# Kernel optimization log

Measured on AMD Instinct MI355X. Metric: run time of the kernel, lower is better.

The kernel has to match this reference:

```python
import jax, jax.numpy as jnp
import numpy as np

DIM = 1024
HEADS = 16
HEAD_DIM = DIM // HEADS
MLP_HID = 4 * DIM
LN_EPS = 1e-5


def layer_norm(x, g, b):
    mu = jnp.mean(x, axis=-1, keepdims=True)
    var = jnp.mean((x - mu) ** 2, axis=-1, keepdims=True)
    return (x - mu) * jax.lax.rsqrt(var + LN_EPS) * g + b


def setup_inputs() -> dict:
    key = jax.random.key(0)
    ks = jax.random.split(key, 8)
    s = 0.02
    return {
        "x": jax.random.normal(ks[0], (8, 1024, DIM), dtype=jnp.float32),
        "attention_mask": jnp.ones((8, 1024), dtype=jnp.int32),
        "ln1_g": jnp.ones((DIM,), jnp.float32),
        "ln1_b": jnp.zeros((DIM,), jnp.float32),
        "qkv_w": jax.random.normal(ks[1], (3 * DIM, DIM), jnp.float32) * s,
        "proj_w": jax.random.normal(ks[2], (DIM, DIM), jnp.float32) * s,
        "proj_b": jnp.zeros((DIM,), jnp.float32),
        "ln2_g": jnp.ones((DIM,), jnp.float32),
        "ln2_b": jnp.zeros((DIM,), jnp.float32),
        "fc1_w": jax.random.normal(ks[3], (MLP_HID, DIM), jnp.float32) * s,
        "fc1_b": jnp.zeros((MLP_HID,), jnp.float32),
        "fc2_w": jax.random.normal(ks[4], (DIM, MLP_HID), jnp.float32) * s,
        "fc2_b": jnp.zeros((DIM,), jnp.float32),
    }


def reference(x, attention_mask, ln1_g, ln1_b, qkv_w, proj_w, proj_b,
              ln2_g, ln2_b, fc1_w, fc1_b, fc2_w, fc2_b):
    B, N, C = x.shape
    scale = HEAD_DIM ** -0.5

    # --- attention branch ---
    h = layer_norm(x, ln1_g, ln1_b)
    qkv = h @ qkv_w.T                       # [B,N,3C] (no qkv bias)
    qkv = qkv.reshape(B, N, 3, HEADS, HEAD_DIM).transpose(2, 0, 3, 1, 4)
    q, k, v = qkv[0], qkv[1], qkv[2]        # each [B,H,N,Dh]
    attn = jnp.einsum('bhnd,bhmd->bhnm', q, k) * scale
    mask = (attention_mask == 0)[:, None, None, :]  # [B,1,1,N]
    attn = jnp.where(mask, -jnp.inf, attn)
    attn = jax.nn.softmax(attn, axis=-1)
    out = jnp.einsum('bhnm,bhmd->bhnd', attn, v)
    out = out.transpose(0, 2, 1, 3).reshape(B, N, C)
    out = out @ proj_w.T + proj_b
    x = x + out

    # --- MLP branch ---
    h = layer_norm(x, ln2_g, ln2_b)
    h = jax.nn.gelu(h @ fc1_w.T + fc1_b, approximate=False)
    h = h @ fc2_w.T + fc2_b
    return x + h
```

## Files before the change

### kernel.cpp

```cpp
#include <hip/hip_runtime.h>
#include <hip/hip_bf16.h>
#include <stdint.h>
#include <math.h>

#define DIMC 1024
#define SEQ 1024
#define NBATCH 8
#define NHEADS 16
#define HDIM 64
#define MLPHID 4096
#define NROWS (NBATCH*SEQ)

typedef __attribute__((ext_vector_type(8))) short short8;
typedef __attribute__((ext_vector_type(4))) float f32x4;
typedef __attribute__((ext_vector_type(16))) float f32x16;
typedef __attribute__((ext_vector_type(4))) unsigned int u32x4;

__device__ __forceinline__ short f2bf(float f) {
  union { float f; uint32_t u; } x; x.f = f;
  uint32_t r = (x.u + 0x7FFFu + ((x.u >> 16) & 1u)) >> 16;
  return (short)r;
}

__device__ __forceinline__ unsigned int pk2(float lo, float hi_) {
  return ((unsigned int)(unsigned short)f2bf(hi_) << 16) |
          (unsigned int)(unsigned short)f2bf(lo);
}

__device__ __forceinline__ float gelu_f(float v) {
  const float t = v * v;
  const float p = fmaf(t, 0.044715f, 1.0f);
  const float e = exp2f(2.3022082f * v * p);
  return v - v * __builtin_amdgcn_rcpf(e + 1.0f);
}

__device__ __forceinline__ f32x4 mfma16(short8 a, short8 b, f32x4 c) {
  return __builtin_amdgcn_mfma_f32_16x16x32_bf16(a, b, c, 0, 0, 0);
}
__device__ __forceinline__ f32x16 mfma32(short8 a, short8 b, f32x16 c) {
  return __builtin_amdgcn_mfma_f32_32x32x16_bf16(a, b, c, 0, 0, 0);
}

__device__ __forceinline__ void gload16(const void* g, void* l) {
  __builtin_amdgcn_global_load_lds(
      (const __attribute__((address_space(1))) uint32_t*)g,
      (__attribute__((address_space(3))) uint32_t*)l, 16, 0, 0);
}

__global__ __launch_bounds__(256)
void f2bw_kernel(const float* __restrict__ w0, const float* __restrict__ w1,
                 const float* __restrict__ w2, const float* __restrict__ w3,
                 short* __restrict__ o0, short* __restrict__ o1,
                 short* __restrict__ o2, short* __restrict__ o3) {
  const int i = blockIdx.x * 256 + threadIdx.x;
  const float4* src;
  short4* dst;
  if (i < 786432)       { src = (const float4*)w0 + i;             dst = (short4*)o0 + i; }
  else if (i < 1048576) { src = (const float4*)w1 + (i - 786432);  dst = (short4*)o1 + (i - 786432); }
  else if (i < 2097152) { src = (const float4*)w2 + (i - 1048576); dst = (short4*)o2 + (i - 1048576); }
  else                  { src = (const float4*)w3 + (i - 2097152); dst = (short4*)o3 + (i - 2097152); }
  const float4 v = *src;
  short4 o;
  o.x = f2bf(v.x); o.y = f2bf(v.y); o.z = f2bf(v.z); o.w = f2bf(v.w);
  *dst = o;
}

__global__ __launch_bounds__(256)
void ln_kernel(const float* __restrict__ x, const float* __restrict__ g,
               const float* __restrict__ beta, short* __restrict__ out) {
  const int row = blockIdx.x;
  const int tid = threadIdx.x;
  const float4 v = ((const float4*)(x + (size_t)row * DIMC))[tid];
  float s = v.x + v.y + v.z + v.w;
  float q = v.x*v.x + v.y*v.y + v.z*v.z + v.w*v.w;
#pragma unroll
  for (int o = 32; o > 0; o >>= 1) { s += __shfl_down(s, o); q += __shfl_down(q, o); }
  __shared__ float rs[4], rq[4];
  const int lane = tid & 63, w = tid >> 6;
  if (lane == 0) { rs[w] = s; rq[w] = q; }
  __syncthreads();
  s = rs[0] + rs[1] + rs[2] + rs[3];
  q = rq[0] + rq[1] + rq[2] + rq[3];
  const float mean = s * (1.0f / DIMC);
  const float var = q * (1.0f / DIMC) - mean * mean;
  const float rstd = rsqrtf(var + 1e-5f);
  const float4 gv = ((const float4*)g)[tid];
  const float4 bv = ((const float4*)beta)[tid];
  short4 o4;
  o4.x = f2bf((v.x - mean) * rstd * gv.x + bv.x);
  o4.y = f2bf((v.y - mean) * rstd * gv.y + bv.y);
  o4.z = f2bf((v.z - mean) * rstd * gv.z + bv.z);
  o4.w = f2bf((v.w - mean) * rstd * gv.w + bv.w);
  ((short4*)(out + (size_t)row * DIMC))[tid] = o4;
}


#define NOVM ((void)0)
#define NOST ((void)0)
#define VMC4 asm volatile("s_waitcnt vmcnt(4)" ::: "memory")
#define VMC2 asm volatile("s_waitcnt vmcnt(2)" ::: "memory")

#define SA(DB, H, T) \
  gload16(sA0 + (H)*hstep + (size_t)(T)*64, stb + ((DB)*4 + (H))*16384); \
  gload16(sA1 + (H)*hstep + (size_t)(T)*64, stb + ((DB)*4 + (H))*16384 + 8192)

#define SB(DB, H, T) \
  gload16(sB0 + (H)*hstep + (size_t)(T)*64, stb + ((DB)*4 + 2 + (H))*16384); \
  gload16(sB1 + (H)*hstep + (size_t)(T)*64, stb + ((DB)*4 + 2 + (H))*16384 + 8192)

#define PH(DB, QA, QB, LDA, LDB, STAGE, VM) \
  do { \
    if (LDA) { \
      _Pragma("unroll") \
      for (int mi = 0; mi < 4; ++mi) { \
        _Pragma("unroll") \
        for (int ks = 0; ks < 2; ++ks) \
          af[mi][ks] = *(const short8*)(ard##DB + (((QA)*4 + mi)*2 + ks)*1024); \
      } \
    } \
    if (LDB) { \
      _Pragma("unroll") \
      for (int ni = 0; ni < 2; ++ni) { \
        _Pragma("unroll") \
        for (int ks = 0; ks < 2; ++ks) \
          bfv[QB][ni][ks] = *(const short8*)(brd##DB + (((QB)*2 + ni)*2 + ks)*1024); \
      } \
    } \
    STAGE; \
    __builtin_amdgcn_s_barrier(); \
    asm volatile("s_waitcnt lgkmcnt(0)" ::: "memory"); \
    __builtin_amdgcn_sched_barrier(0); \
    __builtin_amdgcn_s_setprio(1); \
    _Pragma("unroll") \
    for (int ks = 0; ks < 2; ++ks) { \
      _Pragma("unroll") \
      for (int mi = 0; mi < 4; ++mi) { \
        _Pragma("unroll") \
        for (int ni = 0; ni < 2; ++ni) \
          acc[(QA)*4 + mi][(QB)*2 + ni] = \
            mfma16(af[mi][ks], bfv[QB][ni][ks], acc[(QA)*4 + mi][(QB)*2 + ni]); \
      } \
    } \
    __builtin_amdgcn_s_setprio(0); \
    VM; \
    __builtin_amdgcn_s_barrier(); \
  } while (0)

template<bool BIAS, bool GELU, bool RESID, bool OBF16>
__global__ __launch_bounds__(512)
void gemm8p(const short* __restrict__ A, const short* __restrict__ W,
            const float* __restrict__ bias, const float* __restrict__ resid,
            float* __restrict__ outF, short* __restrict__ outB,
            int M, int N, int K, int ntl, int mt8)
{
  __shared__ __align__(16) char lsm[131072];
  const int tid = threadIdx.x;
  const int lane = tid & 63;
  const int w = tid >> 6;
  const int wm = w >> 2;
  const int wn = w & 3;
  const int fr = lane & 15;
  const int fko = (lane >> 4) << 3;

  const int bid = blockIdx.x;
  const int xcd = bid & 7, l = bid >> 3;
  const int bm = (xcd * mt8 + l / ntl) << 8;
  const int bn = (l % ntl) << 8;

  int row_[2], kk_[2];
#pragma unroll
  for (int j = 0; j < 2; ++j) {
    const int s = j * 8 + (tid >> 6);
    const int r16 = (tid & 63) >> 2;
    const int cb = ((tid & 3) << 4) ^ (((tid >> 5) & 1) << 5);
    row_[j] = (s >> 1) * 16 + r16;
    kk_[j]  = (s & 1) * 32 + (cb >> 1);
  }
  const short* sA0 = A + (size_t)(bm + row_[0]) * K + kk_[0];
  const short* sA1 = A + (size_t)(bm + row_[1]) * K + kk_[1];
  const short* sB0 = W + (size_t)(bn + row_[0]) * K + kk_[0];
  const short* sB1 = W + (size_t)(bn + row_[1]) * K + kk_[1];
  const size_t hstep = (size_t)128 * K;
  char* stb = lsm + tid * 16;

  const int lofs = fr * 64 + ((fko << 1) ^ (((fr >> 3) & 1) << 5));
  const char* ard0 = lsm + wm * 16384 + lofs;
  const char* brd0 = lsm + 32768 + (wn >> 1) * 16384 + (wn & 1) * 8192 + lofs;
  const char* ard1 = ard0 + 65536;
  const char* brd1 = brd0 + 65536;

  short8 af[4][2];
  short8 bfv[2][2][2];
  f32x4 acc[8][4] = {};

  SA(0, 0, 0); SA(0, 1, 0);
  SB(0, 0, 0); SB(0, 1, 0);
  SB(1, 0, 1); SB(1, 1, 1);
  VMC4;
  __builtin_amdgcn_s_barrier();

  const int nk = K >> 6;
  const int nit = nk >> 1;
  const int tmask = nk - 1;
  for (int it = 0; it < nit; ++it) {
    const int t1 = 2 * it + 1;
    const int t2 = (2 * it + 2) & tmask;
    const int t3 = (2 * it + 3) & tmask;
    PH(0, 0, 0, 1, 1, SA(1, 0, t1), NOVM);
    PH(0, 0, 1, 0, 1, SA(1, 1, t1), NOVM);
    PH(0, 1, 1, 1, 0, SB(0, 0, t2), NOVM);
    PH(0, 1, 0, 0, 0, SB(0, 1, t2), VMC4);
    PH(1, 0, 0, 1, 1, SA(0, 0, t2), NOVM);
    PH(1, 0, 1, 0, 1, SA(0, 1, t2), NOVM);
    PH(1, 1, 1, 1, 0, SB(1, 0, t3), NOVM);
    PH(1, 1, 0, 0, 0, SB(1, 1, t3), VMC4);
  }

  asm volatile("s_waitcnt vmcnt(0)" ::: "memory");
  __builtin_amdgcn_s_barrier();

  const int orow0 = bm + wm * 128 + ((lane >> 4) << 2);
  const int ocol0 = bn + wn * 64 + fr;
#pragma unroll
  for (int mi = 0; mi < 8; ++mi) {
#pragma unroll
    for (int r = 0; r < 4; ++r) {
      const int row = orow0 + mi * 16 + r;
      const size_t base = (size_t)row * N;
#pragma unroll
      for (int ni = 0; ni < 4; ++ni) {
        const int col = ocol0 + ni * 16;
        float v = acc[mi][ni][r];
        if (BIAS) v += bias[col];
        if (GELU) v = gelu_f(v);
        if (RESID) v += resid[base + col];
        if (OBF16) outB[base + col] = f2bf(v);
        else       outF[base + col] = v;
      }
    }
  }
}

#define SA2(DB, H, T) \
  gload16(sA0 + (H)*hstep + (size_t)(T)*64, stb + ((DB)*3 + (H))*16384); \
  gload16(sA1 + (H)*hstep + (size_t)(T)*64, stb + ((DB)*3 + (H))*16384 + 8192)

#define SB2(DB, T) \
  gload16(sB0 + (size_t)(T)*64, stb + ((DB)*3 + 2)*16384); \
  gload16(sB1 + (size_t)(T)*64, stb + ((DB)*3 + 2)*16384 + 8192)

#define PH2(DB, QA, QB, LDA, LDB, STAGE, VM) \
  do { \
    if (LDA) { \
      _Pragma("unroll") \
      for (int i = 0; i < 2; ++i) { \
        _Pragma("unroll") \
        for (int ks = 0; ks < 2; ++ks) \
          af[i][ks] = *(const short8*)(ard##DB + (((QA)*2 + i)*2 + ks)*1024); \
      } \
    } \
    if (LDB) { \
      _Pragma("unroll") \
      for (int jn = 0; jn < 2; ++jn) { \
        _Pragma("unroll") \
        for (int ks = 0; ks < 2; ++ks) \
          bfv[QB][jn][ks] = *(const short8*)(brd##DB + (((QB)*2 + jn)*2 + ks)*1024); \
      } \
    } \
    STAGE; \
    __builtin_amdgcn_s_barrier(); \
    asm volatile("s_waitcnt lgkmcnt(0)" ::: "memory"); \
    __builtin_amdgcn_sched_barrier(0); \
    __builtin_amdgcn_s_setprio(1); \
    _Pragma("unroll") \
    for (int ks = 0; ks < 2; ++ks) { \
      _Pragma("unroll") \
      for (int i = 0; i < 2; ++i) { \
        _Pragma("unroll") \
        for (int jn = 0; jn < 2; ++jn) \
          acc[(QA)*2 + i][(QB)*2 + jn] = \
            mfma16(af[i][ks], bfv[QB][jn][ks], acc[(QA)*2 + i][(QB)*2 + jn]); \
      } \
    } \
    __builtin_amdgcn_s_setprio(0); \
    VM; \
    __builtin_amdgcn_s_barrier(); \
  } while (0)

template<bool BIAS, bool GELU, bool RESID, bool OBF16>
__global__ __launch_bounds__(512)
void gemm8pn(const short* __restrict__ A, const short* __restrict__ W,
             const float* __restrict__ bias, const float* __restrict__ resid,
             float* __restrict__ outF, short* __restrict__ outB,
             int M, int N, int K, int ntl, int mt8)
{
  __shared__ __align__(16) char lsm[98304];
  const int tid = threadIdx.x;
  const int lane = tid & 63;
  const int w = tid >> 6;
  const int wm = w >> 1;
  const int wn = w & 1;
  const int fr = lane & 15;
  const int fko = (lane >> 4) << 3;

  const int bid = blockIdx.x;
  const int xcd = bid & 7, l = bid >> 3;
  const int bm = (xcd * mt8 + l / ntl) << 8;
  const int bn = (l % ntl) << 7;

  int row_[2], kk_[2];
#pragma unroll
  for (int j = 0; j < 2; ++j) {
    const int s = j * 8 + (tid >> 6);
    const int r16 = (tid & 63) >> 2;
    const int cb = ((tid & 3) << 4) ^ (((tid >> 5) & 1) << 5);
    row_[j] = (s >> 1) * 16 + r16;
    kk_[j]  = (s & 1) * 32 + (cb >> 1);
  }
  const short* sA0 = A + (size_t)(bm + row_[0]) * K + kk_[0];
  const short* sA1 = A + (size_t)(bm + row_[1]) * K + kk_[1];
  const short* sB0 = W + (size_t)(bn + row_[0]) * K + kk_[0];
  const short* sB1 = W + (size_t)(bn + row_[1]) * K + kk_[1];
  const size_t hstep = (size_t)128 * K;
  char* stb = lsm + tid * 16;

  const int lofs = fr * 64 + ((fko << 1) ^ (((fr >> 3) & 1) << 5));
  const char* ard0 = lsm + (wm >> 1) * 16384 + (wm & 1) * 8192 + lofs;
  const char* brd0 = lsm + 32768 + wn * 8192 + lofs;
  const char* ard1 = ard0 + 49152;
  const char* brd1 = brd0 + 49152;

  short8 af[2][2];
  short8 bfv[2][2][2];
  f32x4 acc[4][4] = {};

  SA2(0, 0, 0); SA2(0, 1, 0); SB2(0, 0);
  SB2(1, 1);
  VMC2;
  __builtin_amdgcn_s_barrier();

  const int nk = K >> 6;
  const int nit = nk >> 1;
  const int tmask = nk - 1;
  for (int it = 0; it < nit; ++it) {
    const int t1 = 2 * it + 1;
    const int t2 = (2 * it + 2) & tmask;
    const int t3 = (2 * it + 3) & tmask;
    PH2(0, 0, 0, 1, 1, SA2(1, 0, t1), NOVM);
    PH2(0, 0, 1, 0, 1, SA2(1, 1, t1), NOVM);
    PH2(0, 1, 1, 1, 0, SB2(0, t2),    NOVM);
    PH2(0, 1, 0, 0, 0, NOST,          VMC2);
    PH2(1, 0, 0, 1, 1, SA2(0, 0, t2), NOVM);
    PH2(1, 0, 1, 0, 1, SA2(0, 1, t2), NOVM);
    PH2(1, 1, 1, 1, 0, SB2(1, t3),    NOVM);
    PH2(1, 1, 0, 0, 0, NOST,          VMC2);
  }

  asm volatile("s_waitcnt vmcnt(0)" ::: "memory");
  __builtin_amdgcn_s_barrier();

  const int orow0 = bm + wm * 64 + ((lane >> 4) << 2);
  const int ocol0 = bn + wn * 64 + fr;
#pragma unroll
  for (int mi = 0; mi < 4; ++mi) {
#pragma unroll
    for (int r = 0; r < 4; ++r) {
      const int row = orow0 + mi * 16 + r;
      const size_t base = (size_t)row * N;
#pragma unroll
      for (int ni = 0; ni < 4; ++ni) {
        const int col = ocol0 + ni * 16;
        float v = acc[mi][ni][r];
        if (BIAS) v += bias[col];
        if (GELU) v = gelu_f(v);
        if (RESID) v += resid[base + col];
        if (OBF16) outB[base + col] = f2bf(v);
        else       outF[base + col] = v;
      }
    }
  }
}

__global__ __launch_bounds__(512)
void attn_kernel(const short* __restrict__ qkv, const int* __restrict__ amask,
                 short* __restrict__ out)
{
  __shared__ __align__(16) char lsm[36864];
  char* lsK = lsm;
  char* lsV = lsm + 16384;
  int* lmask = (int*)(lsm + 32768);
  __shared__ int anym;

  const int tid = threadIdx.x;
  const int lane = tid & 63;
  const int w = tid >> 6;
  const int l31 = lane & 31;
  const int hi = lane >> 5;
  const int swz = (l31 & 7) << 4;

  const int swzb = ((blockIdx.x & 7) << 6) | (blockIdx.x >> 3);
  const int qt = swzb & 3;
  const int h = (swzb >> 2) & 15;
  const int b = swzb >> 6;
  const size_t rowbase = (size_t)b * SEQ;
  const short* qkvB = qkv + rowbase * 3072 + h * 64;

  const int mv0 = amask[b * SEQ + tid];
  const int mv1 = amask[b * SEQ + 512 + tid];
  if (tid == 0) anym = 0;
  lmask[tid] = mv0; lmask[tid + 512] = mv1;
  __syncthreads();
  if ((mv0 == 0) || (mv1 == 0)) atomicOr(&anym, 1);

  const int q0 = qt * 256 + w * 32;
  const short* qptr = qkvB + (size_t)(q0 + l31) * 3072;
  short8 qf[4];
#pragma unroll
  for (int ks = 0; ks < 4; ++ks)
    qf[ks] = *(const short8*)(qptr + ks * 16 + hi * 8);

  const int krow = tid >> 3;
  const int kcc = (((tid & 7) * 16) ^ ((krow & 7) << 4)) >> 1;
  const short* gK = qkvB + 1024 + kcc;
  char* ldK = lsK + tid * 16;
  const int vr = tid & 63;
  const int vc0 = (tid >> 6) << 3;
  const short* gV = qkvB + 2048 + vc0;

  gload16(gK + (size_t)krow * 3072, ldK);
  {
    short8 vv0 = *(const short8*)(gV + (size_t)vr * 3072);
#pragma unroll
    for (int j = 0; j < 8; ++j)
      *(short*)(lsV + (vc0 + j) * 128 + ((2 * vr) ^ (j << 4))) = vv0[j];
  }
  __syncthreads();

  f32x16 oacc[2] = {};
  float psum = 0.f;
  const float CE = 0.125f * 1.44269504f;

  for (int c = 0; c < 16; ++c) {
    const int cur = c & 1;
    const char* lKc = lsK + cur * 8192;
    const char* lVc = lsV + cur * 8192;
    const bool pf = (c < 15);
    short8 vv;
    if (pf) {
      const size_t nb_ = (size_t)(c + 1) * 64;
      gload16(gK + (nb_ + krow) * 3072, ldK + (cur ^ 1) * 8192);
      vv = *(const short8*)(gV + (nb_ + vr) * 3072);
    }

    f32x16 pacc[2] = {};
#pragma unroll
    for (int ks = 0; ks < 4; ++ks) {
#pragma unroll
      for (int s = 0; s < 2; ++s) {
        short8 kf = *(const short8*)(lKc + (s * 32 + l31) * 128 +
                                     ((ks * 32 + hi * 16) ^ swz));
        pacc[s] = mfma32(kf, qf[ks], pacc[s]);
      }
    }

    if (pf) {
      char* lVn = lsV + (cur ^ 1) * 8192;
#pragma unroll
      for (int j = 0; j < 8; ++j)
        *(short*)(lVn + (vc0 + j) * 128 + ((2 * vr) ^ (j << 4))) = vv[j];
    }

    if (anym) {
      const int kv0 = c * 64;
#pragma unroll
      for (int s = 0; s < 2; ++s)
#pragma unroll
        for (int r = 0; r < 16; ++r) {
          const int kv = kv0 + 32 * s + (r & 3) + 8 * (r >> 2) + 4 * hi;
          if (lmask[kv] == 0) pacc[s][r] = -1e30f;
        }
    }

    float pe[2][16];
#pragma unroll
    for (int s = 0; s < 2; ++s)
#pragma unroll
      for (int r = 0; r < 16; ++r) {
        const float p = exp2f(pacc[s][r] * CE);
        pe[s][r] = p;
        psum += p;
      }

    short8 pa[4];
#pragma unroll
    for (int ks = 0; ks < 4; ++ks) {
      const int sh = ks >> 1, kb = (ks & 1) << 3;
      const unsigned int aa = pk2(pe[sh][kb + 0], pe[sh][kb + 1]);
      const unsigned int bb = pk2(pe[sh][kb + 4], pe[sh][kb + 5]);
      const unsigned int cc = pk2(pe[sh][kb + 2], pe[sh][kb + 3]);
      const unsigned int dd = pk2(pe[sh][kb + 6], pe[sh][kb + 7]);
      const unsigned int xbb = __shfl_xor(bb, 32);
      const unsigned int xaa = __shfl_xor(aa, 32);
      const unsigned int xdd = __shfl_xor(dd, 32);
      const unsigned int xcc = __shfl_xor(cc, 32);
      u32x4 t;
      t[0] = hi ? xbb : aa;
      t[1] = hi ? xdd : cc;
      t[2] = hi ? bb : xaa;
      t[3] = hi ? dd : xcc;
      pa[ks] = __builtin_bit_cast(short8, t);
    }

#pragma unroll
    for (int nb = 0; nb < 2; ++nb)
#pragma unroll
      for (int ks = 0; ks < 4; ++ks) {
        short8 vf = *(const short8*)(lVc + (nb * 32 + l31) * 128 +
                                     ((ks * 32 + hi * 16) ^ swz));
        oacc[nb] = mfma32(pa[ks], vf, oacc[nb]);
      }

    __syncthreads();
  }

  const float lt = psum + __shfl_xor(psum, 32);
  const size_t orow = rowbase + q0;
#pragma unroll
  for (int r = 0; r < 16; ++r) {
    const int q = (r & 3) + 8 * (r >> 2) + 4 * hi;
    const float linv = 1.0f / __shfl(lt, q);
    short* op = out + (orow + q) * DIMC + h * 64 + l31;
    op[0]  = f2bf(oacc[0][r] * linv);
    op[32] = f2bf(oacc[1][r] * linv);
  }
}

extern "C" void kernel_launch(void* const* d_in, const int* in_sizes, int n_in,
                              void* d_out, int out_size, void* d_ws, size_t ws_size,
                              hipStream_t stream)
{
  const float* x      = (const float*)d_in[0];
  const int*   amask  = (const int*)d_in[1];
  const float* ln1_g  = (const float*)d_in[2];
  const float* ln1_b  = (const float*)d_in[3];
  const float* qkv_w  = (const float*)d_in[4];
  const float* proj_w = (const float*)d_in[5];
  const float* proj_b = (const float*)d_in[6];
  const float* ln2_g  = (const float*)d_in[7];
  const float* ln2_b  = (const float*)d_in[8];
  const float* fc1_w  = (const float*)d_in[9];
  const float* fc1_b  = (const float*)d_in[10];
  const float* fc2_w  = (const float*)d_in[11];
  const float* fc2_b  = (const float*)d_in[12];
  float* out = (float*)d_out;

  char* ws = (char*)d_ws;
  short* wqkv  = (short*)(ws);
  short* wproj = (short*)(ws + 6291456);
  short* wfc1  = (short*)(ws + 8388608);
  short* wfc2  = (short*)(ws + 16777216);
  float* x1    = (float*)(ws + 25165824);
  short* hb    = (short*)(ws + 58720256);
  short* qkvo  = (short*)(ws + 75497472);
  short* attno = (short*)(ws + 125829120);
  short* fc1o  = (short*)(ws + 75497472);

  f2bw_kernel<<<12288, 256, 0, stream>>>(qkv_w, proj_w, fc1_w, fc2_w,
                                         wqkv, wproj, wfc1, wfc2);

  ln_kernel<<<NROWS, 256, 0, stream>>>(x, ln1_g, ln1_b, hb);

  gemm8pn<false, false, false, true><<<768, 512, 0, stream>>>(
      hb, wqkv, nullptr, nullptr, nullptr, qkvo, NROWS, 3 * DIMC, DIMC, 24, 4);

  attn_kernel<<<512, 512, 0, stream>>>(qkvo, amask, attno);

  gemm8pn<true, false, true, false><<<256, 512, 0, stream>>>(
      attno, wproj, proj_b, x, x1, nullptr, NROWS, DIMC, DIMC, 8, 4);

  ln_kernel<<<NROWS, 256, 0, stream>>>(x1, ln2_g, ln2_b, hb);

  gemm8p<true, true, false, true><<<512, 512, 0, stream>>>(
      hb, wfc1, fc1_b, nullptr, nullptr, fc1o, NROWS, MLPHID, DIMC, 16, 4);

  gemm8pn<true, false, true, false><<<256, 512, 0, stream>>>(
      fc1o, wfc2, fc2_b, x1, out, nullptr, NROWS, DIMC, MLPHID, 8, 4);
}
```

Measured before the change: 364.0 us.

## Retile attention to 256-thread blocks, fold softmax scale into QKV GEMM, use hardware pack/swap

The attention kernel now runs 1024 blocks of 256 threads, each covering 128 queries instead of 256, with K/V tile loads split across the smaller thread count. The softmax scale times log2(e) is folded into the Q columns in the QKV GEMM epilogue, so the attention loop can call raw exp2 directly. BF16 packing uses v_cvt_pk_bf16_f32, the half-wave exchange uses v_permlane32_swap instead of four shuffles plus selects, and s_setprio brackets the MFMA sections. Q is now rounded to bf16 after scaling, which slightly changes numerics, and the raw exp2 and rcp builtins may handle edge cases with less accuracy.

```diff
diff --git a/kernel.cpp b/kernel.cpp
--- a/kernel.cpp
+++ b/kernel.cpp
@@ -22,15 +22,16 @@
   return (short)r;
 }
 
-__device__ __forceinline__ unsigned int pk2(float lo, float hi_) {
-  return ((unsigned int)(unsigned short)f2bf(hi_) << 16) |
-          (unsigned int)(unsigned short)f2bf(lo);
+__device__ __forceinline__ unsigned int cvtpk(float lo, float hi_) {
+  unsigned int r;
+  asm("v_cvt_pk_bf16_f32 %0, %1, %2" : "=v"(r) : "v"(lo), "v"(hi_));
+  return r;
 }
 
 __device__ __forceinline__ float gelu_f(float v) {
   const float t = v * v;
   const float p = fmaf(t, 0.044715f, 1.0f);
-  const float e = exp2f(2.3022082f * v * p);
+  const float e = __builtin_amdgcn_exp2f(2.3022082f * v * p);
   return v - v * __builtin_amdgcn_rcpf(e + 1.0f);
 }
 
@@ -93,7 +94,6 @@
   o4.w = f2bf((v.w - mean) * rstd * gv.w + bv.w);
   ((short4*)(out + (size_t)row * DIMC))[tid] = o4;
 }
-
 
 #define NOVM ((void)0)
 #define NOST ((void)0)
@@ -287,7 +287,7 @@
     __builtin_amdgcn_s_barrier(); \
   } while (0)
 
-template<bool BIAS, bool GELU, bool RESID, bool OBF16>
+template<bool BIAS, bool GELU, bool RESID, bool OBF16, bool QSCALE>
 __global__ __launch_bounds__(512)
 void gemm8pn(const short* __restrict__ A, const short* __restrict__ W,
              const float* __restrict__ bias, const float* __restrict__ resid,
@@ -373,6 +373,7 @@
         float v = acc[mi][ni][r];
         if (BIAS) v += bias[col];
         if (GELU) v = gelu_f(v);
+        if (QSCALE) v *= (col < 1024 ? 0.18033688f : 1.0f);
         if (RESID) v += resid[base + col];
         if (OBF16) outB[base + col] = f2bf(v);
         else       outF[base + col] = v;
@@ -381,7 +382,7 @@
   }
 }
 
-__global__ __launch_bounds__(512)
+__global__ __launch_bounds__(256)
 void attn_kernel(const short* __restrict__ qkv, const int* __restrict__ amask,
                  short* __restrict__ out)
 {
@@ -398,21 +399,21 @@
   const int hi = lane >> 5;
   const int swz = (l31 & 7) << 4;
 
-  const int swzb = ((blockIdx.x & 7) << 6) | (blockIdx.x >> 3);
-  const int qt = swzb & 3;
-  const int h = (swzb >> 2) & 15;
-  const int b = swzb >> 6;
+  const int bid = blockIdx.x;
+  const int swzb = ((bid & 7) << 7) | (bid >> 3);
+  const int qt = swzb & 7;
+  const int h = (swzb >> 3) & 15;
+  const int b = swzb >> 7;
   const size_t rowbase = (size_t)b * SEQ;
   const short* qkvB = qkv + rowbase * 3072 + h * 64;
 
-  const int mv0 = amask[b * SEQ + tid];
-  const int mv1 = amask[b * SEQ + 512 + tid];
+  const int4 mv = ((const int4*)(amask + b * SEQ))[tid];
   if (tid == 0) anym = 0;
-  lmask[tid] = mv0; lmask[tid + 512] = mv1;
+  ((int4*)lmask)[tid] = mv;
   __syncthreads();
-  if ((mv0 == 0) || (mv1 == 0)) atomicOr(&anym, 1);
-
-  const int q0 = qt * 256 + w * 32;
+  if ((mv.x & mv.y & mv.z & mv.w) == 0) atomicOr(&anym, 1);
+
+  const int q0 = qt * 128 + w * 32;
   const short* qptr = qkvB + (size_t)(q0 + l31) * 3072;
   short8 qf[4];
 #pragma unroll
@@ -428,31 +429,38 @@
   const short* gV = qkvB + 2048 + vc0;
 
   gload16(gK + (size_t)krow * 3072, ldK);
+  gload16(gK + (size_t)(krow + 32) * 3072, ldK + 4096);
   {
-    short8 vv0 = *(const short8*)(gV + (size_t)vr * 3072);
-#pragma unroll
-    for (int j = 0; j < 8; ++j)
-      *(short*)(lsV + (vc0 + j) * 128 + ((2 * vr) ^ (j << 4))) = vv0[j];
+    short8 a0 = *(const short8*)(gV + (size_t)vr * 3072);
+    short8 a1 = *(const short8*)(gV + (size_t)vr * 3072 + 32);
+#pragma unroll
+    for (int j = 0; j < 8; ++j) {
+      *(short*)(lsV + (vc0 + j) * 128 + ((2 * vr) ^ (j << 4))) = a0[j];
+      *(short*)(lsV + (vc0 + 32 + j) * 128 + ((2 * vr) ^ (j << 4))) = a1[j];
+    }
   }
   __syncthreads();
 
   f32x16 oacc[2] = {};
   float psum = 0.f;
-  const float CE = 0.125f * 1.44269504f;
 
   for (int c = 0; c < 16; ++c) {
     const int cur = c & 1;
     const char* lKc = lsK + cur * 8192;
     const char* lVc = lsV + cur * 8192;
     const bool pf = (c < 15);
-    short8 vv;
+    short8 vv0, vv1;
     if (pf) {
       const size_t nb_ = (size_t)(c + 1) * 64;
-      gload16(gK + (nb_ + krow) * 3072, ldK + (cur ^ 1) * 8192);
-      vv = *(const short8*)(gV + (nb_ + vr) * 3072);
+      char* ldKn = ldK + (cur ^ 1) * 8192;
+      gload16(gK + (nb_ + krow) * 3072, ldKn);
+      gload16(gK + (nb_ + krow + 32) * 3072, ldKn + 4096);
+      vv0 = *(const short8*)(gV + (nb_ + vr) * 3072);
+      vv1 = *(const short8*)(gV + (nb_ + vr) * 3072 + 32);
     }
 
     f32x16 pacc[2] = {};
+    __builtin_amdgcn_s_setprio(1);
 #pragma unroll
     for (int ks = 0; ks < 4; ++ks) {
 #pragma unroll
@@ -462,12 +470,15 @@
         pacc[s] = mfma32(kf, qf[ks], pacc[s]);
       }
     }
+    __builtin_amdgcn_s_setprio(0);
 
     if (pf) {
       char* lVn = lsV + (cur ^ 1) * 8192;
 #pragma unroll
-      for (int j = 0; j < 8; ++j)
-        *(short*)(lVn + (vc0 + j) * 128 + ((2 * vr) ^ (j << 4))) = vv[j];
+      for (int j = 0; j < 8; ++j) {
+        *(short*)(lVn + (vc0 + j) * 128 + ((2 * vr) ^ (j << 4))) = vv0[j];
+        *(short*)(lVn + (vc0 + 32 + j) * 128 + ((2 * vr) ^ (j << 4))) = vv1[j];
+      }
     }
 
     if (anym) {
@@ -486,7 +497,7 @@
     for (int s = 0; s < 2; ++s)
 #pragma unroll
       for (int r = 0; r < 16; ++r) {
-        const float p = exp2f(pacc[s][r] * CE);
+        const float p = __builtin_amdgcn_exp2f(pacc[s][r]);
         pe[s][r] = p;
         psum += p;
       }
@@ -495,22 +506,18 @@
 #pragma unroll
     for (int ks = 0; ks < 4; ++ks) {
       const int sh = ks >> 1, kb = (ks & 1) << 3;
-      const unsigned int aa = pk2(pe[sh][kb + 0], pe[sh][kb + 1]);
-      const unsigned int bb = pk2(pe[sh][kb + 4], pe[sh][kb + 5]);
-      const unsigned int cc = pk2(pe[sh][kb + 2], pe[sh][kb + 3]);
-      const unsigned int dd = pk2(pe[sh][kb + 6], pe[sh][kb + 7]);
-      const unsigned int xbb = __shfl_xor(bb, 32);
-      const unsigned int xaa = __shfl_xor(aa, 32);
-      const unsigned int xdd = __shfl_xor(dd, 32);
-      const unsigned int xcc = __shfl_xor(cc, 32);
+      unsigned int aa = cvtpk(pe[sh][kb + 0], pe[sh][kb + 1]);
+      unsigned int bb = cvtpk(pe[sh][kb + 4], pe[sh][kb + 5]);
+      unsigned int cc = cvtpk(pe[sh][kb + 2], pe[sh][kb + 3]);
+      unsigned int dd = cvtpk(pe[sh][kb + 6], pe[sh][kb + 7]);
+      asm volatile("v_permlane32_swap_b32 %0, %1" : "+v"(aa), "+v"(bb));
+      asm volatile("v_permlane32_swap_b32 %0, %1" : "+v"(cc), "+v"(dd));
       u32x4 t;
-      t[0] = hi ? xbb : aa;
-      t[1] = hi ? xdd : cc;
-      t[2] = hi ? bb : xaa;
-      t[3] = hi ? dd : xcc;
+      t[0] = aa; t[1] = cc; t[2] = bb; t[3] = dd;
       pa[ks] = __builtin_bit_cast(short8, t);
     }
 
+    __builtin_amdgcn_s_setprio(1);
 #pragma unroll
     for (int nb = 0; nb < 2; ++nb)
 #pragma unroll
@@ -519,6 +526,7 @@
                                      ((ks * 32 + hi * 16) ^ swz));
         oacc[nb] = mfma32(pa[ks], vf, oacc[nb]);
       }
+    __builtin_amdgcn_s_setprio(0);
 
     __syncthreads();
   }
@@ -570,12 +578,12 @@
 
   ln_kernel<<<NROWS, 256, 0, stream>>>(x, ln1_g, ln1_b, hb);
 
-  gemm8pn<false, false, false, true><<<768, 512, 0, stream>>>(
+  gemm8pn<false, false, false, true, true><<<768, 512, 0, stream>>>(
       hb, wqkv, nullptr, nullptr, nullptr, qkvo, NROWS, 3 * DIMC, DIMC, 24, 4);
 
-  attn_kernel<<<512, 512, 0, stream>>>(qkvo, amask, attno);
-
-  gemm8pn<true, false, true, false><<<256, 512, 0, stream>>>(
+  attn_kernel<<<1024, 256, 0, stream>>>(qkvo, amask, attno);
+
+  gemm8pn<true, false, true, false, false><<<256, 512, 0, stream>>>(
       attno, wproj, proj_b, x, x1, nullptr, NROWS, DIMC, DIMC, 8, 4);
 
   ln_kernel<<<NROWS, 256, 0, stream>>>(x1, ln2_g, ln2_b, hb);
@@ -583,6 +591,6 @@
   gemm8p<true, true, false, true><<<512, 512, 0, stream>>>(
       hb, wfc1, fc1_b, nullptr, nullptr, fc1o, NROWS, MLPHID, DIMC, 16, 4);
 
-  gemm8pn<true, false, true, false><<<256, 512, 0, stream>>>(
+  gemm8pn<true, false, true, false, false><<<256, 512, 0, stream>>>(
       fc1o, wfc2, fc2_b, x1, out, nullptr, NROWS, DIMC, MLPHID, 8, 4);
 }
```

Result: faster. 327.1 us (-10.1%).
